# Optimization experiments

Hardware: AMD Instinct MI355X
Metric: run time of the kernel (lower is better)

## Reference

```python
import jax, jax.numpy as jnp
import numpy as np

SEQ, EMBED, VOCAB = 2048, 128, 50257

def setup_inputs() -> dict:
    key = jax.random.key(0)
    ks = jax.random.split(key, 6)
    return {
        "psi_real": jax.random.normal(ks[0], (SEQ, EMBED), dtype=jnp.float32),
        "psi_imag": jax.random.normal(ks[1], (SEQ, EMBED), dtype=jnp.float32),
        # original: torch.randn(vocab, embed, complex64) * 0.1
        "patterns_real": jax.random.normal(ks[2], (VOCAB, EMBED), dtype=jnp.float32) * 0.1,
        "patterns_imag": jax.random.normal(ks[3], (VOCAB, EMBED), dtype=jnp.float32) * 0.1,
        # nn.Linear(embed, vocab): W [vocab, embed], b [vocab]
        "W": jax.random.normal(ks[4], (VOCAB, EMBED), dtype=jnp.float32) * (1.0 / np.sqrt(EMBED)),
        "b": jax.random.normal(ks[5], (VOCAB,), dtype=jnp.float32) * 0.01,
    }

def reference(psi_real, psi_imag, patterns_real, patterns_imag, W, b):
    psi = jax.lax.complex(psi_real, psi_imag)            # [S, E] complex
    patterns = jax.lax.complex(patterns_real, patterns_imag)  # [V, E] complex
    # torch.vdot(psi[i], pattern_j) = sum(conj(psi[i]) * pattern_j)
    # -> batched: conj(psi) @ patterns.T, then |.|^2
    scores = jnp.einsum('se,ve->sv', jnp.conj(psi), patterns)  # [S, V] complex
    interference_logits = (scores.real ** 2 + scores.imag ** 2).astype(jnp.float32)
    linear_logits = psi_real @ W.T + b                    # Linear on psi.real
    return interference_logits + linear_logits
```

## Files before the change

kernel.cpp:

```cpp
#include <hip/hip_runtime.h>

static constexpr int S  = 2048;
static constexpr int E  = 128;
static constexpr int V  = 50257;

static constexpr int MB = 128;
static constexpr int NB = 48;
static constexpr int KC = 32;
static constexpr int KP = 40;

typedef __attribute__((ext_vector_type(8))) short bf16x8;
typedef __attribute__((ext_vector_type(4))) float floatx4;

#define MF(a, b, c) __builtin_amdgcn_mfma_f32_16x16x32_bf16((a), (b), (c), 0, 0, 0)

__device__ __forceinline__ void split2(float x, unsigned short& hi, unsigned short& lo) {
    unsigned xb = __float_as_uint(x);
    hi = (unsigned short)(xb >> 16);
    float hf = __uint_as_float(xb & 0xFFFF0000u);
    lo = (unsigned short)(__float_as_uint(x - hf) >> 16);
}

__global__ __launch_bounds__(256, 2)
void interference_kernel(const float* __restrict__ psi_r,
                         const float* __restrict__ psi_i,
                         const float* __restrict__ pat_r,
                         const float* __restrict__ pat_i,
                         const float* __restrict__ Wm,
                         const float* __restrict__ bias,
                         float* __restrict__ out)
{
    __shared__ short smem[4 * MB * KP + 6 * NB * KP];
    short* sA = smem;
    short* sB = smem + 4 * MB * KP;

    const int tid  = threadIdx.x;
    const int wave = tid >> 6;
    const int lane = tid & 63;
    const int quad = lane >> 4;
    const int r16  = lane & 15;

    const int m0 = blockIdx.y * MB;
    const int v0 = blockIdx.x * NB;

    floatx4 Cr[2][3], Ci[2][3], Cl[2][3];
    #pragma unroll
    for (int mi = 0; mi < 2; mi++)
        #pragma unroll
        for (int ni = 0; ni < 3; ni++) {
            Cr[mi][ni] = floatx4{0.f, 0.f, 0.f, 0.f};
            Ci[mi][ni] = floatx4{0.f, 0.f, 0.f, 0.f};
            Cl[mi][ni] = floatx4{0.f, 0.f, 0.f, 0.f};
        }

    for (int chunk = 0; chunk < E / KC; chunk++) {
        const int kc = chunk * KC;

        #pragma unroll
        for (int i = 0; i < 8; i++) {
            int idx = tid + i * 256;
            int src = idx >> 10;
            int rem = idx & 1023;
            int row = rem >> 3;
            int kq  = rem & 7;
            const float* bsrc = src ? psi_i : psi_r;
            const float4 x = *(const float4*)(bsrc + (m0 + row) * E + kc + kq * 4);
            unsigned short h0, h1, h2, h3, l0, l1, l2, l3;
            split2(x.x, h0, l0); split2(x.y, h1, l1);
            split2(x.z, h2, l2); split2(x.w, h3, l3);
            int offh = ((src * 2) * MB + row) * KP + kq * 4;
            int offl = offh + MB * KP;
            uint2 uh = make_uint2((unsigned)h0 | ((unsigned)h1 << 16),
                                  (unsigned)h2 | ((unsigned)h3 << 16));
            uint2 ul = make_uint2((unsigned)l0 | ((unsigned)l1 << 16),
                                  (unsigned)l2 | ((unsigned)l3 << 16));
            *(uint2*)(sA + offh) = uh;
            *(uint2*)(sA + offl) = ul;
        }

        #pragma unroll
        for (int i = 0; i < 5; i++) {
            int idx = tid + i * 256;
            if (idx < 1152) {
                int src = idx / 384;
                int rem = idx - src * 384;
                int row = rem >> 3;
                int kq  = rem & 7;
                int vv  = v0 + row; if (vv > V - 1) vv = V - 1;
                const float* bsrc = (src == 0) ? pat_r : ((src == 1) ? pat_i : Wm);
                const float4 x = *(const float4*)(bsrc + vv * E + kc + kq * 4);
                unsigned short h0, h1, h2, h3, l0, l1, l2, l3;
                split2(x.x, h0, l0); split2(x.y, h1, l1);
                split2(x.z, h2, l2); split2(x.w, h3, l3);
                int offh = ((src * 2) * NB + row) * KP + kq * 4;
                int offl = offh + NB * KP;
                uint2 uh = make_uint2((unsigned)h0 | ((unsigned)h1 << 16),
                                      (unsigned)h2 | ((unsigned)h3 << 16));
                uint2 ul = make_uint2((unsigned)l0 | ((unsigned)l1 << 16),
                                      (unsigned)l2 | ((unsigned)l3 << 16));
                *(uint2*)(sB + offh) = uh;
                *(uint2*)(sB + offl) = ul;
            }
        }
        __syncthreads();

        bf16x8 fB[6][3];
        #pragma unroll
        for (int bm = 0; bm < 6; bm++)
            #pragma unroll
            for (int ni = 0; ni < 3; ni++)
                fB[bm][ni] = *(const bf16x8*)(sB + (bm * NB + ni * 16 + r16) * KP + quad * 8);

        #pragma unroll
        for (int mi = 0; mi < 2; mi++) {
            const int ab = (wave * 32 + mi * 16 + r16) * KP + quad * 8;
            bf16x8 Prh = *(const bf16x8*)(sA + ab);
            bf16x8 Prl = *(const bf16x8*)(sA + ab + MB * KP);
            bf16x8 Pih = *(const bf16x8*)(sA + ab + 2 * MB * KP);
            bf16x8 Pil = *(const bf16x8*)(sA + ab + 3 * MB * KP);
            #pragma unroll
            for (int ni = 0; ni < 3; ni++) {
                Cr[mi][ni] = MF(Prh, fB[0][ni], Cr[mi][ni]);
                Cr[mi][ni] = MF(Prh, fB[1][ni], Cr[mi][ni]);
                Cr[mi][ni] = MF(Prl, fB[0][ni], Cr[mi][ni]);
                Cr[mi][ni] = MF(Pih, fB[2][ni], Cr[mi][ni]);
                Cr[mi][ni] = MF(Pih, fB[3][ni], Cr[mi][ni]);
                Cr[mi][ni] = MF(Pil, fB[2][ni], Cr[mi][ni]);
                Ci[mi][ni] = MF(Prh, fB[2][ni], Ci[mi][ni]);
                Ci[mi][ni] = MF(Prh, fB[3][ni], Ci[mi][ni]);
                Ci[mi][ni] = MF(Prl, fB[2][ni], Ci[mi][ni]);
                Cl[mi][ni] = MF(Prh, fB[4][ni], Cl[mi][ni]);
                Cl[mi][ni] = MF(Prh, fB[5][ni], Cl[mi][ni]);
                Cl[mi][ni] = MF(Prl, fB[4][ni], Cl[mi][ni]);
            }
            Pih = Pih ^ (short)0x8000;
            Pil = Pil ^ (short)0x8000;
            #pragma unroll
            for (int ni = 0; ni < 3; ni++) {
                Ci[mi][ni] = MF(Pih, fB[0][ni], Ci[mi][ni]);
                Ci[mi][ni] = MF(Pih, fB[1][ni], Ci[mi][ni]);
                Ci[mi][ni] = MF(Pil, fB[0][ni], Ci[mi][ni]);
            }
        }
        __syncthreads();
    }

    #pragma unroll
    for (int ni = 0; ni < 3; ni++) {
        const int col = v0 + ni * 16 + r16;
        if (col < V) {
            const float bv = bias[col];
            #pragma unroll
            for (int mi = 0; mi < 2; mi++) {
                const int rbase = m0 + wave * 32 + mi * 16 + quad * 4;
                #pragma unroll
                for (int r = 0; r < 4; r++) {
                    float cr = Cr[mi][ni][r];
                    float ci = Ci[mi][ni][r];
                    float cl = Cl[mi][ni][r];
                    out[(long)(rbase + r) * V + col] = cr * cr + ci * ci + cl + bv;
                }
            }
        }
    }
}

extern "C" void kernel_launch(void* const* d_in, const int* in_sizes, int n_in,
                              void* d_out, int out_size, void* d_ws, size_t ws_size,
                              hipStream_t stream) {
    const float* psi_r = (const float*)d_in[0];
    const float* psi_i = (const float*)d_in[1];
    const float* pat_r = (const float*)d_in[2];
    const float* pat_i = (const float*)d_in[3];
    const float* Wm    = (const float*)d_in[4];
    const float* b     = (const float*)d_in[5];
    float* out = (float*)d_out;

    dim3 grid((V + NB - 1) / NB, S / MB);
    interference_kernel<<<grid, dim3(256), 0, stream>>>(psi_r, psi_i, pat_r, pat_i, Wm, b, out);
}
```

Baseline: 962.1 us.

## Precompute bf16 hi/lo splits into fragment-ordered workspace and drop LDS staging

```diff
diff --git a/kernel.cpp b/kernel.cpp
--- a/kernel.cpp
+++ b/kernel.cpp
@@ -4,15 +4,18 @@
 static constexpr int E  = 128;
 static constexpr int V  = 50257;
 
-static constexpr int MB = 128;
-static constexpr int NB = 48;
-static constexpr int KC = 32;
-static constexpr int KP = 40;
-
 typedef __attribute__((ext_vector_type(8))) short bf16x8;
 typedef __attribute__((ext_vector_type(4))) float floatx4;
 
 #define MF(a, b, c) __builtin_amdgcn_mfma_f32_16x16x32_bf16((a), (b), (c), 0, 0, 0)
+
+static constexpr int  RT       = S / 16;
+static constexpr int  NBLK     = (V + 63) / 64;
+static constexpr int  CT       = NBLK * 4;
+static constexpr long A_MAT    = (long)RT * 4 * 64 * 8;
+static constexpr long B_MAT    = (long)CT * 4 * 64 * 8;
+static constexpr long WS_SHORTS = 4 * A_MAT + 6 * B_MAT;
+static constexpr long WS_BYTES  = WS_SHORTS * 2;
 
 __device__ __forceinline__ void split2(float x, unsigned short& hi, unsigned short& lo) {
     unsigned xb = __float_as_uint(x);
@@ -20,6 +23,173 @@
     float hf = __uint_as_float(xb & 0xFFFF0000u);
     lo = (unsigned short)(__float_as_uint(x - hf) >> 16);
 }
+
+__device__ __forceinline__ void cvt8(const float* v, bf16x8& hi, bf16x8& lo) {
+    #pragma unroll
+    for (int j = 0; j < 8; j++) {
+        unsigned short h, l;
+        split2(v[j], h, l);
+        hi[j] = (short)h;
+        lo[j] = (short)l;
+    }
+}
+
+__global__ __launch_bounds__(256)
+void pre_a(const float* __restrict__ psi_r, const float* __restrict__ psi_i,
+           short* __restrict__ ws)
+{
+    const int t    = blockIdx.x * 256 + threadIdx.x;
+    const int lane = t & 63;
+    const int kc   = (t >> 6) & 3;
+    const int rt   = t >> 8;
+    const int row  = rt * 16 + (lane & 15);
+    const int k0   = kc * 32 + (lane >> 4) * 8;
+
+    float v[8];
+    const float* p = psi_r + (long)row * E + k0;
+    #pragma unroll
+    for (int j = 0; j < 8; j++) v[j] = p[j];
+    bf16x8 hi, lo; cvt8(v, hi, lo);
+    *(bf16x8*)(ws + 0 * A_MAT + (long)t * 8) = hi;
+    *(bf16x8*)(ws + 1 * A_MAT + (long)t * 8) = lo;
+
+    p = psi_i + (long)row * E + k0;
+    #pragma unroll
+    for (int j = 0; j < 8; j++) v[j] = p[j];
+    cvt8(v, hi, lo);
+    *(bf16x8*)(ws + 2 * A_MAT + (long)t * 8) = hi;
+    *(bf16x8*)(ws + 3 * A_MAT + (long)t * 8) = lo;
+}
+
+__global__ __launch_bounds__(256)
+void pre_b(const float* __restrict__ pat_r, const float* __restrict__ pat_i,
+           const float* __restrict__ Wm, short* __restrict__ ws)
+{
+    const int t    = blockIdx.x * 256 + threadIdx.x;
+    const int lane = t & 63;
+    const int kc   = (t >> 6) & 3;
+    const int ct   = t >> 8;
+    const int row  = ct * 16 + (lane & 15);
+    const int k0   = kc * 32 + (lane >> 4) * 8;
+    const bool ok  = row < V;
+
+    short* B0 = ws + 4 * A_MAT;
+    const float* srcs[3] = { pat_r, pat_i, Wm };
+    #pragma unroll
+    for (int s = 0; s < 3; s++) {
+        float v[8];
+        if (ok) {
+            const float* p = srcs[s] + (long)row * E + k0;
+            #pragma unroll
+            for (int j = 0; j < 8; j++) v[j] = p[j];
+        } else {
+            #pragma unroll
+            for (int j = 0; j < 8; j++) v[j] = 0.f;
+        }
+        bf16x8 hi, lo; cvt8(v, hi, lo);
+        *(bf16x8*)(B0 + (long)(2 * s)     * B_MAT + (long)t * 8) = hi;
+        *(bf16x8*)(B0 + (long)(2 * s + 1) * B_MAT + (long)t * 8) = lo;
+    }
+}
+
+__global__ __launch_bounds__(256, 2)
+void interference_mfma(const short* __restrict__ ws,
+                       const float* __restrict__ bias,
+                       float* __restrict__ out)
+{
+    const int tid  = threadIdx.x;
+    const int wave = tid >> 6;
+    const int lane = tid & 63;
+    const int quad = lane >> 4;
+    const int r16  = lane & 15;
+    const int wm   = wave >> 1;
+    const int wn   = wave & 1;
+    const int mb   = blockIdx.x;
+    const int nb   = blockIdx.y;
+
+    const short* Ah = ws + 0 * A_MAT;
+    const short* Al = ws + 1 * A_MAT;
+    const short* Ih = ws + 2 * A_MAT;
+    const short* Il = ws + 3 * A_MAT;
+    const short* Bm = ws + 4 * A_MAT;
+
+    const int rt0 = mb * 8 + wm * 4;
+    const int ct0 = nb * 4 + wn * 2;
+
+    floatx4 Cr[4][2], Ci[4][2], Cl[4][2];
+    #pragma unroll
+    for (int mi = 0; mi < 4; mi++)
+        #pragma unroll
+        for (int ni = 0; ni < 2; ni++) {
+            Cr[mi][ni] = floatx4{0.f, 0.f, 0.f, 0.f};
+            Ci[mi][ni] = floatx4{0.f, 0.f, 0.f, 0.f};
+            Cl[mi][ni] = floatx4{0.f, 0.f, 0.f, 0.f};
+        }
+
+    for (int kc = 0; kc < 4; kc++) {
+        bf16x8 fB[6][2];
+        #pragma unroll
+        for (int m = 0; m < 6; m++)
+            #pragma unroll
+            for (int ni = 0; ni < 2; ni++)
+                fB[m][ni] = *(const bf16x8*)(Bm + (long)m * B_MAT +
+                                             (((long)(ct0 + ni) * 4 + kc) * 64 + lane) * 8);
+        #pragma unroll
+        for (int mi = 0; mi < 4; mi++) {
+            const long ao = (((long)(rt0 + mi) * 4 + kc) * 64 + lane) * 8;
+            bf16x8 ah = *(const bf16x8*)(Ah + ao);
+            bf16x8 al = *(const bf16x8*)(Al + ao);
+            bf16x8 ih = *(const bf16x8*)(Ih + ao);
+            bf16x8 il = *(const bf16x8*)(Il + ao);
+            #pragma unroll
+            for (int ni = 0; ni < 2; ni++) {
+                Cr[mi][ni] = MF(ah, fB[0][ni], Cr[mi][ni]);
+                Cr[mi][ni] = MF(ah, fB[1][ni], Cr[mi][ni]);
+                Cr[mi][ni] = MF(al, fB[0][ni], Cr[mi][ni]);
+                Cr[mi][ni] = MF(ih, fB[2][ni], Cr[mi][ni]);
+                Cr[mi][ni] = MF(ih, fB[3][ni], Cr[mi][ni]);
+                Cr[mi][ni] = MF(il, fB[2][ni], Cr[mi][ni]);
+                Ci[mi][ni] = MF(ah, fB[2][ni], Ci[mi][ni]);
+                Ci[mi][ni] = MF(ah, fB[3][ni], Ci[mi][ni]);
+                Ci[mi][ni] = MF(al, fB[2][ni], Ci[mi][ni]);
+                Cl[mi][ni] = MF(ah, fB[4][ni], Cl[mi][ni]);
+                Cl[mi][ni] = MF(ah, fB[5][ni], Cl[mi][ni]);
+                Cl[mi][ni] = MF(al, fB[4][ni], Cl[mi][ni]);
+            }
+            ih = ih ^ (short)0x8000;
+            il = il ^ (short)0x8000;
+            #pragma unroll
+            for (int ni = 0; ni < 2; ni++) {
+                Ci[mi][ni] = MF(ih, fB[0][ni], Ci[mi][ni]);
+                Ci[mi][ni] = MF(ih, fB[1][ni], Ci[mi][ni]);
+                Ci[mi][ni] = MF(il, fB[0][ni], Ci[mi][ni]);
+            }
+        }
+    }
+
+    #pragma unroll
+    for (int ni = 0; ni < 2; ni++) {
+        const int col = nb * 64 + wn * 32 + ni * 16 + r16;
+        if (col < V) {
+            const float bv = bias[col];
+            #pragma unroll
+            for (int mi = 0; mi < 4; mi++) {
+                const int rbase = mb * 128 + wm * 64 + mi * 16 + quad * 4;
+                #pragma unroll
+                for (int r = 0; r < 4; r++) {
+                    float cr = Cr[mi][ni][r];
+                    float ci = Ci[mi][ni][r];
+                    float cl = Cl[mi][ni][r];
+                    out[(long)(rbase + r) * V + col] = cr * cr + ci * ci + cl + bv;
+                }
+            }
+        }
+    }
+}
+
+static constexpr int MB = 128;
+static constexpr int NB = 48;
+static constexpr int KP = 40;
 
 __global__ __launch_bounds__(256, 2)
 void interference_kernel(const float* __restrict__ psi_r,
@@ -53,9 +223,8 @@
             Cl[mi][ni] = floatx4{0.f, 0.f, 0.f, 0.f};
         }
 
-    for (int chunk = 0; chunk < E / KC; chunk++) {
-        const int kc = chunk * KC;
-
+    for (int chunk = 0; chunk < E / 32; chunk++) {
+        const int kc = chunk * 32;
         #pragma unroll
         for (int i = 0; i < 8; i++) {
             int idx = tid + i * 256;
@@ -77,7 +246,6 @@
             *(uint2*)(sA + offh) = uh;
             *(uint2*)(sA + offl) = ul;
         }
-
         #pragma unroll
         for (int i = 0; i < 5; i++) {
             int idx = tid + i * 256;
@@ -176,6 +344,13 @@
     const float* b     = (const float*)d_in[5];
     float* out = (float*)d_out;
 
-    dim3 grid((V + NB - 1) / NB, S / MB);
-    interference_kernel<<<grid, dim3(256), 0, stream>>>(psi_r, psi_i, pat_r, pat_i, Wm, b, out);
-}
+    if (d_ws && ws_size >= (size_t)WS_BYTES) {
+        short* ws = (short*)d_ws;
+        pre_a<<<RT * 4 * 64 / 256, 256, 0, stream>>>(psi_r, psi_i, ws);
+        pre_b<<<CT * 4 * 64 / 256, 256, 0, stream>>>(pat_r, pat_i, Wm, ws);
+        interference_mfma<<<dim3(S / 128, NBLK), 256, 0, stream>>>(ws, b, out);
+    } else {
+        dim3 grid((V + NB - 1) / NB, S / MB);
+        interference_kernel<<<grid, dim3(256), 0, stream>>>(psi_r, psi_i, pat_r, pat_i, Wm, b, out);
+    }
+}
```

After: 804.0 us. -16.4%, faster.
